# Kernel tuning notes

Hardware: AMD Instinct MI355X
Metric: run time of the kernel (lower is better)

The kernel has to match this reference:

```python
import jax, jax.numpy as jnp
import numpy as np

VOCAB = 50257
D = 1024
EDGES = [0, 20000, 40000, VOCAB]  # cluster boundaries
HSZ = [1024, 256, 64]             # D // 4**i per cluster


def setup_inputs() -> dict:
    key = jax.random.key(0)
    ks = jax.random.split(key, 8)
    emb_input = jax.random.randint(ks[0], (8, 2048), 0, VOCAB, dtype=jnp.int64)
    inp = {"emb_input": emb_input}
    for i in range(3):
        vsz = EDGES[i + 1] - EDGES[i]
        h = HSZ[i]
        inp[f"emb{i}"] = jax.random.normal(ks[1 + 2 * i], (vsz, h), dtype=jnp.float32) * 0.02
        # nn.Linear(h, D, bias=False) weight has shape [D, h]
        inp[f"w{i}"] = jax.random.normal(ks[2 + 2 * i], (D, h), dtype=jnp.float32) * 0.02
    return inp


def reference(emb_input, emb0, w0, emb1, w1, emb2, w2):
    B, S = emb_input.shape
    idx = emb_input.reshape(-1)  # [N]
    clusters = [(emb0, w0), (emb1, w1), (emb2, w2)]
    out = jnp.zeros((idx.shape[0], D), dtype=jnp.float32)
    for i, (emb, w) in enumerate(clusters):
        lo, hi = EDGES[i], EDGES[i + 1]
        mask = (idx >= lo) & (idx < hi)                       # [N]
        local = jnp.clip(idx - lo, 0, emb.shape[0] - 1)       # in-range gather ids
        h = emb[local]                                        # [N, hsz_i]
        proj = jnp.einsum('nh,dh->nd', h, w)                  # [N, D]
        out = out + jnp.where(mask[:, None], proj, 0.0)
    return out.reshape(B, S, D)
```

## Files before the change

kernel.cpp:

```cpp
#include <hip/hip_runtime.h>
#include <stdint.h>

#define DOUT 1024
#define NMAX 16384

typedef __attribute__((ext_vector_type(8))) short short8;
typedef __attribute__((ext_vector_type(4))) float floatx4;

__device__ __forceinline__ unsigned short f2bf(float f) {
  union { float f; uint32_t u; } v;
  v.f = f;
  return (unsigned short)((v.u + 0x7FFFu + ((v.u >> 16) & 1u)) >> 16);
}

__global__ __launch_bounds__(256) void classify_cvt_kernel(
    const int* __restrict__ idx, int* __restrict__ cnt,
    int* __restrict__ bucket, int* __restrict__ blocal, int N,
    const float* __restrict__ w0, const float* __restrict__ w1,
    const float* __restrict__ w2, unsigned short* __restrict__ wb0,
    unsigned short* __restrict__ wb1, unsigned short* __restrict__ wb2) {
  if (blockIdx.x < 64) {
    int n = blockIdx.x * 256 + threadIdx.x;
    int lane = threadIdx.x & 63;
    int c = -1, v = 0;
    if (n < N) {
      v = idx[n];
      c = (v < 20000) ? 0 : ((v < 40000) ? 1 : 2);
    }
#pragma unroll
    for (int k = 0; k < 3; ++k) {
      unsigned long long m = __ballot(c == k);
      if (c == k) {
        int leader = __ffsll((unsigned long long)m) - 1;
        int base = 0;
        if (lane == leader) base = atomicAdd(&cnt[k], (int)__popcll(m));
        base = __shfl(base, leader);
        int rank = (int)__popcll(m & ((1ull << (unsigned)lane) - 1ull));
        int lo = (k == 0) ? 0 : (k == 1) ? 20000 : 40000;
        bucket[k * NMAX + base + rank] = n;
        blocal[k * NMAX + base + rank] = v - lo;
      }
    }
  } else {
    int i = (blockIdx.x - 64) * 256 + threadIdx.x;
    if (i >= 344064) return;
    const float4* src;
    ushort4* dst;
    if (i < 262144) {
      src = (const float4*)w0 + i;
      dst = (ushort4*)wb0 + i;
    } else if (i < 327680) {
      src = (const float4*)w1 + (i - 262144);
      dst = (ushort4*)wb1 + (i - 262144);
    } else {
      src = (const float4*)w2 + (i - 327680);
      dst = (ushort4*)wb2 + (i - 327680);
    }
    float4 v = *src;
    ushort4 o;
    o.x = f2bf(v.x); o.y = f2bf(v.y); o.z = f2bf(v.z); o.w = f2bf(v.w);
    *dst = o;
  }
}

__global__ __launch_bounds__(256) void gather_fused(
    const float* __restrict__ emb0, const float* __restrict__ emb1,
    const float* __restrict__ emb2, const int* __restrict__ blocal,
    const int* __restrict__ cnt, unsigned short* __restrict__ a0,
    unsigned short* __restrict__ a1, unsigned short* __restrict__ a2) {
  const int z = blockIdx.z;
  const int hshift = 10 - 2 * z;
  const float* emb = (z == 0) ? emb0 : (z == 1) ? emb1 : emb2;
  unsigned short* acomp = (z == 0) ? a0 : (z == 1) ? a1 : a2;
  const int* bl = blocal + z * NMAX;
  const int count = cnt[z];
  const int h4s = hshift - 2;
  const int total = count << h4s;
  for (int i = blockIdx.x * 256 + threadIdx.x; i < total; i += gridDim.x * 256) {
    int row = i >> h4s;
    int k4 = i & ((1 << h4s) - 1);
    int loc = bl[row];
    float4 v = ((const float4*)(emb + ((size_t)loc << hshift)))[k4];
    ushort4 o;
    o.x = f2bf(v.x); o.y = f2bf(v.y); o.z = f2bf(v.z); o.w = f2bf(v.w);
    ((ushort4*)(acomp + ((size_t)row << hshift)))[k4] = o;
  }
}

template <int H>
__device__ __forceinline__ void gemm_body(
    const unsigned short* __restrict__ A, const unsigned short* __restrict__ B,
    int count, const int* __restrict__ bucket, float* __restrict__ out,
    unsigned short* As, unsigned short* Bs, int* rowTok) {
  const int m0 = blockIdx.y * 128;
  if (m0 >= count) return;
  const int n0 = blockIdx.x * 128;

  const int tid = threadIdx.x;
  const int wave = tid >> 6;
  const int lane = tid & 63;
  const int quad = lane >> 4;
  const int l16 = lane & 15;
  const int wm = wave & 1;
  const int wn = wave >> 1;

  if (tid < 128) {
    int m = m0 + tid;
    rowTok[tid] = (m < count) ? bucket[m] : -1;
  }

  floatx4 acc[4][4];
#pragma unroll
  for (int i = 0; i < 4; ++i)
#pragma unroll
    for (int j = 0; j < 4; ++j) acc[i][j] = (floatx4){0.f, 0.f, 0.f, 0.f};

  const char* Ab = (const char*)A;
  const char* Bb = (const char*)B;
  const int row_lo = tid >> 2;
  const int ck = tid & 3;

  for (int k0 = 0; k0 < H; k0 += 32) {
    __syncthreads();
#pragma unroll
    for (int p = 0; p < 2; ++p) {
      const int row = p * 64 + row_lo;
      const void* ga = Ab + ((size_t)(m0 + row) * H + k0) * 2 + ck * 16;
      const void* gb = Bb + ((size_t)(n0 + row) * H + k0) * 2 + ck * 16;
      void* la = (char*)As + (p * 4096 + wave * 1024);
      void* lb = (char*)Bs + (p * 4096 + wave * 1024);
      __builtin_amdgcn_global_load_lds(
          (const __attribute__((address_space(1))) void*)ga,
          (__attribute__((address_space(3))) void*)la, 16, 0, 0);
      __builtin_amdgcn_global_load_lds(
          (const __attribute__((address_space(1))) void*)gb,
          (__attribute__((address_space(3))) void*)lb, 16, 0, 0);
    }
    __syncthreads();

    short8 af[4], bf[4];
#pragma unroll
    for (int mi = 0; mi < 4; ++mi)
      af[mi] = *(const short8*)&As[(wm * 64 + mi * 16 + l16) * 32 + quad * 8];
#pragma unroll
    for (int ni = 0; ni < 4; ++ni)
      bf[ni] = *(const short8*)&Bs[(wn * 64 + ni * 16 + l16) * 32 + quad * 8];
#pragma unroll
    for (int mi = 0; mi < 4; ++mi)
#pragma unroll
      for (int ni = 0; ni < 4; ++ni)
        acc[mi][ni] = __builtin_amdgcn_mfma_f32_16x16x32_bf16(
            af[mi], bf[ni], acc[mi][ni], 0, 0, 0);
  }

  const int colBase = n0 + wn * 64 + l16;
#pragma unroll
  for (int mi = 0; mi < 4; ++mi) {
#pragma unroll
    for (int r = 0; r < 4; ++r) {
      int tok = rowTok[wm * 64 + mi * 16 + quad * 4 + r];
      if (tok >= 0) {
        float* o = out + (size_t)tok * DOUT + colBase;
#pragma unroll
        for (int ni = 0; ni < 4; ++ni) o[ni * 16] = acc[mi][ni][r];
      }
    }
  }
}

__global__ __launch_bounds__(256) void gemm_fused(
    const unsigned short* __restrict__ a0, const unsigned short* __restrict__ a1,
    const unsigned short* __restrict__ a2, const unsigned short* __restrict__ wb0,
    const unsigned short* __restrict__ wb1, const unsigned short* __restrict__ wb2,
    const int* __restrict__ cnt, const int* __restrict__ bucket,
    float* __restrict__ out) {
  __shared__ __align__(16) unsigned short As[128 * 32];
  __shared__ __align__(16) unsigned short Bs[128 * 32];
  __shared__ int rowTok[128];

  const int z = blockIdx.z;
  if (z == 0)
    gemm_body<1024>(a0, wb0, cnt[0], bucket + 0 * NMAX, out, As, Bs, rowTok);
  else if (z == 1)
    gemm_body<256>(a1, wb1, cnt[1], bucket + 1 * NMAX, out, As, Bs, rowTok);
  else
    gemm_body<64>(a2, wb2, cnt[2], bucket + 2 * NMAX, out, As, Bs, rowTok);
}

extern "C" void kernel_launch(void* const* d_in, const int* in_sizes, int n_in,
                              void* d_out, int out_size, void* d_ws, size_t ws_size,
                              hipStream_t stream) {
  const int* idx = (const int*)d_in[0];
  const float* emb0 = (const float*)d_in[1];
  const float* w0 = (const float*)d_in[2];
  const float* emb1 = (const float*)d_in[3];
  const float* w1 = (const float*)d_in[4];
  const float* emb2 = (const float*)d_in[5];
  const float* w2 = (const float*)d_in[6];
  float* out = (float*)d_out;
  const int N = in_sizes[0];

  char* ws = (char*)d_ws;
  int* cnt = (int*)ws;
  int* bucket = (int*)(ws + 1024);
  int* blocal = bucket + 3 * NMAX;
  size_t off = 1024 + (size_t)6 * NMAX * 4;
  off = (off + 255) & ~(size_t)255;
  unsigned short* wb0 = (unsigned short*)(ws + off); off += (size_t)DOUT * 1024 * 2;
  unsigned short* wb1 = (unsigned short*)(ws + off); off += (size_t)DOUT * 256 * 2;
  unsigned short* wb2 = (unsigned short*)(ws + off); off += (size_t)DOUT * 64 * 2;
  off = (off + 255) & ~(size_t)255;
  unsigned short* a0 = (unsigned short*)(ws + off); off += (size_t)NMAX * 1024 * 2;
  unsigned short* a1 = (unsigned short*)(ws + off); off += (size_t)NMAX * 256 * 2;
  unsigned short* a2 = (unsigned short*)(ws + off); off += (size_t)NMAX * 64 * 2;

  hipMemsetAsync(cnt, 0, 16 * sizeof(int), stream);

  classify_cvt_kernel<<<64 + 1344, 256, 0, stream>>>(
      idx, cnt, bucket, blocal, N, w0, w1, w2, wb0, wb1, wb2);

  dim3 ggrid(512, 1, 3);
  gather_fused<<<ggrid, 256, 0, stream>>>(emb0, emb1, emb2, blocal, cnt, a0, a1, a2);

  dim3 grid(DOUT / 128, NMAX / 128, 3);
  gemm_fused<<<grid, 256, 0, stream>>>(a0, a1, a2, wb0, wb1, wb2, cnt, bucket, out);
}
```

Before: 213.8 us.

## Pre-swizzle A and B into MFMA fragment layout and drop LDS staging in GEMM

The weight-conversion and gather kernels now write bf16 data directly in a per-lane MFMA fragment order, so each wave can load its 16x32 fragments straight from global memory with 16-byte loads. The GEMM no longer stages tiles through shared memory or uses barriers. Instead it software-pipelines register fragment loads one K-step ahead, and it reads token ids from global at store time. This removes the LDS round trip and the syncs, but it relies on L2 for the reuse that shared memory used to provide. It also sets an occupancy hint of 3 blocks per CU.

```diff
diff --git a/kernel.cpp b/kernel.cpp
--- a/kernel.cpp
+++ b/kernel.cpp
@@ -1,4 +1,5 @@
 #include <hip/hip_runtime.h>
+#include <hip/hip_bf16.h>
 #include <stdint.h>
 
 #define DOUT 1024
@@ -11,6 +12,30 @@
   union { float f; uint32_t u; } v;
   v.f = f;
   return (unsigned short)((v.u + 0x7FFFu + ((v.u >> 16) & 1u)) >> 16);
+}
+
+__device__ __forceinline__ short8 cvt8(float4 a, float4 b) {
+  __hip_bfloat162 p0 = __float22bfloat162_rn(make_float2(a.x, a.y));
+  __hip_bfloat162 p1 = __float22bfloat162_rn(make_float2(a.z, a.w));
+  __hip_bfloat162 p2 = __float22bfloat162_rn(make_float2(b.x, b.y));
+  __hip_bfloat162 p3 = __float22bfloat162_rn(make_float2(b.z, b.w));
+  union { __hip_bfloat162 h[4]; short8 s; } u;
+  u.h[0] = p0; u.h[1] = p1; u.h[2] = p2; u.h[3] = p3;
+  return u.s;
+}
+
+template <int H>
+__device__ __forceinline__ void cvtB_swz(const float* __restrict__ w,
+                                         unsigned short* __restrict__ dst, int u) {
+  constexpr int C = H / 32;
+  int l = u & 63;
+  int rest = u >> 6;
+  int c = rest & (C - 1);
+  int nt = rest / C;
+  const float* s = w + (size_t)(nt * 16 + (l & 15)) * H + c * 32 + ((l >> 4) << 3);
+  float4 v0 = *(const float4*)s;
+  float4 v1 = *(const float4*)(s + 4);
+  *(short8*)(dst + (((size_t)nt * C + c) * 64 + l) * 8) = cvt8(v0, v1);
 }
 
 __global__ __launch_bounds__(256) void classify_cvt_kernel(
@@ -43,55 +68,46 @@
     }
   } else {
     int i = (blockIdx.x - 64) * 256 + threadIdx.x;
-    if (i >= 344064) return;
-    const float4* src;
-    ushort4* dst;
-    if (i < 262144) {
-      src = (const float4*)w0 + i;
-      dst = (ushort4*)wb0 + i;
-    } else if (i < 327680) {
-      src = (const float4*)w1 + (i - 262144);
-      dst = (ushort4*)wb1 + (i - 262144);
-    } else {
-      src = (const float4*)w2 + (i - 327680);
-      dst = (ushort4*)wb2 + (i - 327680);
-    }
-    float4 v = *src;
-    ushort4 o;
-    o.x = f2bf(v.x); o.y = f2bf(v.y); o.z = f2bf(v.z); o.w = f2bf(v.w);
-    *dst = o;
-  }
-}
-
-__global__ __launch_bounds__(256) void gather_fused(
+    if (i < 131072) cvtB_swz<1024>(w0, wb0, i);
+    else if (i < 163840) cvtB_swz<256>(w1, wb1, i - 131072);
+    else if (i < 172032) cvtB_swz<64>(w2, wb2, i - 163840);
+  }
+}
+
+__global__ __launch_bounds__(256) void gather_swz(
     const float* __restrict__ emb0, const float* __restrict__ emb1,
     const float* __restrict__ emb2, const int* __restrict__ blocal,
     const int* __restrict__ cnt, unsigned short* __restrict__ a0,
     unsigned short* __restrict__ a1, unsigned short* __restrict__ a2) {
   const int z = blockIdx.z;
-  const int hshift = 10 - 2 * z;
+  const int H = (z == 0) ? 1024 : (z == 1) ? 256 : 64;
+  const int lc = (z == 0) ? 5 : (z == 1) ? 3 : 1;
+  const int C = 1 << lc;
   const float* emb = (z == 0) ? emb0 : (z == 1) ? emb1 : emb2;
-  unsigned short* acomp = (z == 0) ? a0 : (z == 1) ? a1 : a2;
+  unsigned short* asw = (z == 0) ? a0 : (z == 1) ? a1 : a2;
   const int* bl = blocal + z * NMAX;
   const int count = cnt[z];
-  const int h4s = hshift - 2;
-  const int total = count << h4s;
+  const int mtiles = (count + 15) >> 4;
+  const int total = (mtiles << lc) << 6;
   for (int i = blockIdx.x * 256 + threadIdx.x; i < total; i += gridDim.x * 256) {
-    int row = i >> h4s;
-    int k4 = i & ((1 << h4s) - 1);
-    int loc = bl[row];
-    float4 v = ((const float4*)(emb + ((size_t)loc << hshift)))[k4];
-    ushort4 o;
-    o.x = f2bf(v.x); o.y = f2bf(v.y); o.z = f2bf(v.z); o.w = f2bf(v.w);
-    ((ushort4*)(acomp + ((size_t)row << hshift)))[k4] = o;
+    int l = i & 63;
+    int rest = i >> 6;
+    int c = rest & (C - 1);
+    int mt = rest >> lc;
+    int m = (mt << 4) + (l & 15);
+    int loc = (m < count) ? bl[m] : 0;
+    const float* s = emb + (size_t)loc * H + (c << 5) + ((l >> 4) << 3);
+    float4 v0 = *(const float4*)s;
+    float4 v1 = *(const float4*)(s + 4);
+    *(short8*)(asw + (((size_t)(mt << lc) + c) * 64 + l) * 8) = cvt8(v0, v1);
   }
 }
 
 template <int H>
 __device__ __forceinline__ void gemm_body(
-    const unsigned short* __restrict__ A, const unsigned short* __restrict__ B,
-    int count, const int* __restrict__ bucket, float* __restrict__ out,
-    unsigned short* As, unsigned short* Bs, int* rowTok) {
+    const unsigned short* __restrict__ Asw, const unsigned short* __restrict__ Bsw,
+    int count, const int* __restrict__ bucket, float* __restrict__ out) {
+  constexpr int C = H / 32;
   const int m0 = blockIdx.y * 128;
   if (m0 >= count) return;
   const int n0 = blockIdx.x * 128;
@@ -104,10 +120,10 @@
   const int wm = wave & 1;
   const int wn = wave >> 1;
 
-  if (tid < 128) {
-    int m = m0 + tid;
-    rowTok[tid] = (m < count) ? bucket[m] : -1;
-  }
+  const unsigned short* abase =
+      Asw + (((size_t)(m0 / 16 + wm * 4) * C) * 64 + lane) * 8;
+  const unsigned short* bbase =
+      Bsw + (((size_t)(n0 / 16 + wn * 4) * C) * 64 + lane) * 8;
 
   floatx4 acc[4][4];
 #pragma unroll
@@ -115,50 +131,43 @@
 #pragma unroll
     for (int j = 0; j < 4; ++j) acc[i][j] = (floatx4){0.f, 0.f, 0.f, 0.f};
 
-  const char* Ab = (const char*)A;
-  const char* Bb = (const char*)B;
-  const int row_lo = tid >> 2;
-  const int ck = tid & 3;
-
-  for (int k0 = 0; k0 < H; k0 += 32) {
-    __syncthreads();
-#pragma unroll
-    for (int p = 0; p < 2; ++p) {
-      const int row = p * 64 + row_lo;
-      const void* ga = Ab + ((size_t)(m0 + row) * H + k0) * 2 + ck * 16;
-      const void* gb = Bb + ((size_t)(n0 + row) * H + k0) * 2 + ck * 16;
-      void* la = (char*)As + (p * 4096 + wave * 1024);
-      void* lb = (char*)Bs + (p * 4096 + wave * 1024);
-      __builtin_amdgcn_global_load_lds(
-          (const __attribute__((address_space(1))) void*)ga,
-          (__attribute__((address_space(3))) void*)la, 16, 0, 0);
-      __builtin_amdgcn_global_load_lds(
-          (const __attribute__((address_space(1))) void*)gb,
-          (__attribute__((address_space(3))) void*)lb, 16, 0, 0);
-    }
-    __syncthreads();
-
-    short8 af[4], bf[4];
-#pragma unroll
-    for (int mi = 0; mi < 4; ++mi)
-      af[mi] = *(const short8*)&As[(wm * 64 + mi * 16 + l16) * 32 + quad * 8];
-#pragma unroll
-    for (int ni = 0; ni < 4; ++ni)
-      bf[ni] = *(const short8*)&Bs[(wn * 64 + ni * 16 + l16) * 32 + quad * 8];
+  short8 curA[4], curB[4], nxtA[4], nxtB[4];
+#pragma unroll
+  for (int f = 0; f < 4; ++f) {
+    curA[f] = *(const short8*)(abase + (size_t)f * C * 512);
+    curB[f] = *(const short8*)(bbase + (size_t)f * C * 512);
+  }
+
+#pragma unroll 2
+  for (int c = 0; c < C - 1; ++c) {
+#pragma unroll
+    for (int f = 0; f < 4; ++f) {
+      nxtA[f] = *(const short8*)(abase + ((size_t)f * C + c + 1) * 512);
+      nxtB[f] = *(const short8*)(bbase + ((size_t)f * C + c + 1) * 512);
+    }
 #pragma unroll
     for (int mi = 0; mi < 4; ++mi)
 #pragma unroll
       for (int ni = 0; ni < 4; ++ni)
         acc[mi][ni] = __builtin_amdgcn_mfma_f32_16x16x32_bf16(
-            af[mi], bf[ni], acc[mi][ni], 0, 0, 0);
-  }
+            curA[mi], curB[ni], acc[mi][ni], 0, 0, 0);
+#pragma unroll
+    for (int f = 0; f < 4; ++f) { curA[f] = nxtA[f]; curB[f] = nxtB[f]; }
+  }
+#pragma unroll
+  for (int mi = 0; mi < 4; ++mi)
+#pragma unroll
+    for (int ni = 0; ni < 4; ++ni)
+      acc[mi][ni] = __builtin_amdgcn_mfma_f32_16x16x32_bf16(
+          curA[mi], curB[ni], acc[mi][ni], 0, 0, 0);
 
   const int colBase = n0 + wn * 64 + l16;
 #pragma unroll
   for (int mi = 0; mi < 4; ++mi) {
 #pragma unroll
     for (int r = 0; r < 4; ++r) {
-      int tok = rowTok[wm * 64 + mi * 16 + quad * 4 + r];
+      int m = m0 + wm * 64 + mi * 16 + quad * 4 + r;
+      int tok = (m < count) ? bucket[m] : -1;
       if (tok >= 0) {
         float* o = out + (size_t)tok * DOUT + colBase;
 #pragma unroll
@@ -168,23 +177,19 @@
   }
 }
 
-__global__ __launch_bounds__(256) void gemm_fused(
+__global__ __launch_bounds__(256, 3) void gemm_nolds(
     const unsigned short* __restrict__ a0, const unsigned short* __restrict__ a1,
     const unsigned short* __restrict__ a2, const unsigned short* __restrict__ wb0,
     const unsigned short* __restrict__ wb1, const unsigned short* __restrict__ wb2,
     const int* __restrict__ cnt, const int* __restrict__ bucket,
     float* __restrict__ out) {
-  __shared__ __align__(16) unsigned short As[128 * 32];
-  __shared__ __align__(16) unsigned short Bs[128 * 32];
-  __shared__ int rowTok[128];
-
   const int z = blockIdx.z;
   if (z == 0)
-    gemm_body<1024>(a0, wb0, cnt[0], bucket + 0 * NMAX, out, As, Bs, rowTok);
+    gemm_body<1024>(a0, wb0, cnt[0], bucket + 0 * NMAX, out);
   else if (z == 1)
-    gemm_body<256>(a1, wb1, cnt[1], bucket + 1 * NMAX, out, As, Bs, rowTok);
+    gemm_body<256>(a1, wb1, cnt[1], bucket + 1 * NMAX, out);
   else
-    gemm_body<64>(a2, wb2, cnt[2], bucket + 2 * NMAX, out, As, Bs, rowTok);
+    gemm_body<64>(a2, wb2, cnt[2], bucket + 2 * NMAX, out);
 }
 
 extern "C" void kernel_launch(void* const* d_in, const int* in_sizes, int n_in,
@@ -216,12 +221,12 @@
 
   hipMemsetAsync(cnt, 0, 16 * sizeof(int), stream);
 
-  classify_cvt_kernel<<<64 + 1344, 256, 0, stream>>>(
+  classify_cvt_kernel<<<64 + 672, 256, 0, stream>>>(
       idx, cnt, bucket, blocal, N, w0, w1, w2, wb0, wb1, wb2);
 
-  dim3 ggrid(512, 1, 3);
-  gather_fused<<<ggrid, 256, 0, stream>>>(emb0, emb1, emb2, blocal, cnt, a0, a1, a2);
+  dim3 ggrid(1024, 1, 3);
+  gather_swz<<<ggrid, 256, 0, stream>>>(emb0, emb1, emb2, blocal, cnt, a0, a1, a2);
 
   dim3 grid(DOUT / 128, NMAX / 128, 3);
-  gemm_fused<<<grid, 256, 0, stream>>>(a0, a1, a2, wb0, wb1, wb2, cnt, bucket, out);
-}
+  gemm_nolds<<<grid, 256, 0, stream>>>(a0, a1, a2, wb0, wb1, wb2, cnt, bucket, out);
+}
```

Result: no change. 212.6 us (-0.6%).
